# Kernel tuning notes

Hardware: AMD Instinct MI355X
Metric: run time of the kernel (lower is better)

The kernel has to match this reference:

```python
import jax, jax.numpy as jnp
import numpy as np

B, T, D, H, K, M = 2, 2048, 1024, 16, 3, 16384
HD = D // H
SCALE = D * (H ** 0.5)  # faithful to source: n_embd / n_head**(-0.5)


def _normalize(v, axis=-1, eps=1e-12):
    # torch F.normalize: v / max(||v||, eps)
    n = jnp.sqrt(jnp.sum(v * v, axis=axis, keepdims=True))
    return v / jnp.maximum(n, eps)


def setup_inputs() -> dict:
    key = jax.random.key(0)
    ks = jax.random.split(key, 12)
    s = 1.0 / np.sqrt(D)
    return {
        "x": jax.random.normal(ks[0], (B, T, D), jnp.float32),
        "Wq": jax.random.normal(ks[1], (D, D), jnp.float32) * s,
        "bq": jax.random.normal(ks[2], (D,), jnp.float32) * 0.01,
        "Wk": jax.random.normal(ks[3], (D, D), jnp.float32) * s,
        "bk": jax.random.normal(ks[4], (D,), jnp.float32) * 0.01,
        "Wv": jax.random.normal(ks[5], (D, D), jnp.float32) * s,
        "bv": jax.random.normal(ks[6], (D,), jnp.float32) * 0.01,
        "Wo": jax.random.normal(ks[7], (D, D), jnp.float32) * s,
        "bo": jax.random.normal(ks[8], (D,), jnp.float32) * 0.01,
        "gate_bias": jax.random.normal(ks[9], (H, 1, 1), jnp.float32),
        "mem_bank": jax.random.normal(ks[10], (B, M, 2, D), jnp.float32) * s,
        "knn_idx": jax.random.randint(ks[11], (B, T, K), 0, M, jnp.int32),
    }


def reference(x, Wq, bq, Wk, bk, Wv, bv, Wo, bo, gate_bias, mem_bank, knn_idx):
    b, t, d = x.shape
    # projections + L2-normalize q,k (as in source)
    q = _normalize(x @ Wq.T + bq)
    k = _normalize(x @ Wk.T + bk)
    v = x @ Wv.T + bv
    # split heads: b t (h hd) -> b h t hd
    q = q.reshape(b, t, H, HD).transpose(0, 2, 1, 3)
    k = k.reshape(b, t, H, HD).transpose(0, 2, 1, 3)
    v = v.reshape(b, t, H, HD).transpose(0, 2, 1, 3)
    # local causal attention (hand-rolled, dropout is eval no-op)
    qk = jnp.einsum('bhid,bhjd->bhij', q, k) * SCALE  # [b,h,t,t]
    causal = jnp.triu(jnp.ones((t, t), dtype=bool), 1)
    qk = jnp.where(causal, -jnp.inf, qk)
    attn = jax.nn.softmax(qk, axis=-1)
    qkv = jnp.einsum('bhij,bhjd->bhid', attn, v)  # [b,h,t,hd]
    # kNN memory retrieval: gather top-k (key,value) memories per token
    mem = mem_bank[jnp.arange(b)[:, None, None], knn_idx]  # [b,t,k,2,D]
    mem_k = mem[..., 0, :].reshape(b, t, K, H, HD).transpose(0, 3, 1, 2, 4)  # [b,h,t,k,hd]
    mem_v = mem[..., 1, :].reshape(b, t, K, H, HD).transpose(0, 3, 1, 2, 4)
    mem_qk = jnp.einsum('bhtd,bhtkd->bhtk', q.astype(jnp.float32), mem_k) * SCALE
    mem_attn = jax.nn.softmax(mem_qk, axis=-1)
    mem_qkv = jnp.einsum('bhtk,bhtkd->bhtd', mem_attn, mem_v)
    # per-head gated blend, bf16 round-trip (source casts to bfloat16)
    combined = mem_qkv * gate_bias + qkv * (1.0 - gate_bias)  # gate [H,1,1] broadcasts
    combined = combined.astype(jnp.bfloat16).astype(jnp.float32)
    y = combined.transpose(0, 2, 1, 3).reshape(b, t, d)  # b h t hd -> b t D
    return y @ Wo.T + bo
```

## Files before the change

kernel.cpp:

```cpp
#include <hip/hip_runtime.h>
#include <math.h>

#define B_ 2
#define T_ 2048
#define D_ 1024
#define H_ 16
#define HD_ 64
#define M_ 16384
#define SCALE_F 4096.0f
#define LDP 3072
#define ST 72

using short8 = __attribute__((ext_vector_type(8))) short;
using bf16x8 = __attribute__((ext_vector_type(8))) __bf16;
using f32x4  = __attribute__((ext_vector_type(4))) float;

__device__ __forceinline__ unsigned short f2bf(float x){
  unsigned u = __builtin_bit_cast(unsigned, x);
  u += 0x7fffu + ((u >> 16) & 1u);
  return (unsigned short)(u >> 16);
}
__device__ __forceinline__ float bf2f(unsigned short h){
  unsigned u = ((unsigned)h) << 16;
  return __builtin_bit_cast(float, u);
}
__device__ __forceinline__ float bfround(float x){ return bf2f(f2bf(x)); }

__device__ __forceinline__ float wsum(float v){
  #pragma unroll
  for (int off = 32; off; off >>= 1) v += __shfl_xor(v, off);
  return v;
}

__device__ __forceinline__ void ld_g2l16(const unsigned short* g, unsigned short* l){
  __builtin_amdgcn_global_load_lds(
      (const __attribute__((address_space(1))) void*)g,
      (__attribute__((address_space(3))) void*)l, 16, 0, 0);
}

__global__ __launch_bounds__(256)
void cvt_all(const float* __restrict__ x, const float* __restrict__ Wq,
             const float* __restrict__ Wk, const float* __restrict__ Wv,
             const float* __restrict__ Wo,
             unsigned short* __restrict__ Xhi, unsigned short* __restrict__ Xlo,
             unsigned short* __restrict__ Whi, unsigned short* __restrict__ Wlo,
             unsigned short* __restrict__ Wohi)
{
  const int i = blockIdx.x*256 + threadIdx.x;
  const float* src; unsigned short* hi; unsigned short* lo = nullptr; int rel;
  if      (i < 1048576){ src = x;  hi = Xhi;            lo = Xlo;            rel = i; }
  else if (i < 1310720){ src = Wq; hi = Whi;            lo = Wlo;            rel = i - 1048576; }
  else if (i < 1572864){ src = Wk; hi = Whi + 1048576;  lo = Wlo + 1048576;  rel = i - 1310720; }
  else if (i < 1835008){ src = Wv; hi = Whi + 2097152;                       rel = i - 1572864; }
  else                 { src = Wo; hi = Wohi;                                rel = i - 1835008; }
  float4 v = *(const float4*)(src + (size_t)rel*4);
  unsigned short h0=f2bf(v.x), h1=f2bf(v.y), h2=f2bf(v.z), h3=f2bf(v.w);
  uint2 hh; hh.x = (unsigned)h0 | ((unsigned)h1 << 16);
            hh.y = (unsigned)h2 | ((unsigned)h3 << 16);
  *(uint2*)(hi + (size_t)rel*4) = hh;
  if (lo){
    uint2 ll;
    ll.x = (unsigned)f2bf(v.x-bf2f(h0)) | ((unsigned)f2bf(v.y-bf2f(h1)) << 16);
    ll.y = (unsigned)f2bf(v.z-bf2f(h2)) | ((unsigned)f2bf(v.w-bf2f(h3)) << 16);
    *(uint2*)(lo + (size_t)rel*4) = ll;
  }
}

template<bool COMP>
__global__ __launch_bounds__(256)
void gemm_lds(const unsigned short* __restrict__ Ahi_g, const unsigned short* __restrict__ Alo_g,
              const unsigned short* __restrict__ Bhi_g, const unsigned short* __restrict__ Blo_g,
              const float* __restrict__ bias0, const float* __restrict__ bias1,
              const float* __restrict__ bias2,
              float* __restrict__ C, int ldc)
{
  __shared__ __align__(16) unsigned short Ah[128*32];
  __shared__ __align__(16) unsigned short Bh[128*32];
  __shared__ __align__(16) unsigned short Al[COMP ? 128*32 : 8];
  __shared__ __align__(16) unsigned short Bl[COMP ? 128*32 : 8];

  const int tid = threadIdx.x, lane = tid & 63, wv = tid >> 6;
  const int wm = wv >> 1, wn = wv & 1;
  const int mi = lane & 15, quad = lane >> 4;
  const int n0 = blockIdx.x * 128;
  const int m0 = blockIdx.y * 128;
  const int seg = n0 >> 10;
  const float* bias = (seg == 0) ? bias0 : (seg == 1) ? bias1 : bias2;
  const int nw = n0 & 1023;
  const bool comp = COMP && (seg < 2);

  f32x4 acc[4][4];
  #pragma unroll
  for (int a = 0; a < 4; ++a)
    #pragma unroll
    for (int b = 0; b < 4; ++b)
      acc[a][b] = (f32x4){0.f, 0.f, 0.f, 0.f};

  for (int k0 = 0; k0 < 1024; k0 += 32){
    __syncthreads();
    #pragma unroll
    for (int t = 0; t < 2; ++t){
      int j = wv*128 + t*64 + lane;
      int row = j >> 2, c16 = j & 3;
      size_t ga = (size_t)(m0 + row)*1024 + k0 + c16*8;
      size_t gb = (size_t)(n0 + row)*1024 + k0 + c16*8;
      ld_g2l16(Ahi_g + ga, Ah + j*8);
      ld_g2l16(Bhi_g + gb, Bh + j*8);
      if (comp){
        ld_g2l16(Alo_g + ga, Al + j*8);
        ld_g2l16(Blo_g + gb, Bl + j*8);
      }
    }
    __syncthreads();

    bf16x8 ah[4], al[4];
    #pragma unroll
    for (int a = 0; a < 4; ++a){
      int r = wm*64 + a*16 + mi;
      ah[a] = __builtin_bit_cast(bf16x8, *(const short8*)(Ah + r*32 + quad*8));
      if (comp)
        al[a] = __builtin_bit_cast(bf16x8, *(const short8*)(Al + r*32 + quad*8));
    }
    #pragma unroll
    for (int b = 0; b < 4; ++b){
      int r = wn*64 + b*16 + mi;
      bf16x8 bh = __builtin_bit_cast(bf16x8, *(const short8*)(Bh + r*32 + quad*8));
      if (comp){
        bf16x8 bl = __builtin_bit_cast(bf16x8, *(const short8*)(Bl + r*32 + quad*8));
        #pragma unroll
        for (int a = 0; a < 4; ++a){
          acc[a][b] = __builtin_amdgcn_mfma_f32_16x16x32_bf16(al[a], bh, acc[a][b], 0, 0, 0);
          acc[a][b] = __builtin_amdgcn_mfma_f32_16x16x32_bf16(ah[a], bl, acc[a][b], 0, 0, 0);
          acc[a][b] = __builtin_amdgcn_mfma_f32_16x16x32_bf16(ah[a], bh, acc[a][b], 0, 0, 0);
        }
      } else {
        #pragma unroll
        for (int a = 0; a < 4; ++a)
          acc[a][b] = __builtin_amdgcn_mfma_f32_16x16x32_bf16(ah[a], bh, acc[a][b], 0, 0, 0);
      }
    }
  }
  #pragma unroll
  for (int a = 0; a < 4; ++a)
    #pragma unroll
    for (int b = 0; b < 4; ++b)
      #pragma unroll
      for (int r = 0; r < 4; ++r){
        int row  = m0 + wm*64 + a*16 + quad*4 + r;
        int coll = wn*64 + b*16 + mi;
        C[(size_t)row*ldc + n0 + coll] = acc[a][b][r] + bias[nw + coll];
      }
}

__global__ __launch_bounds__(256)
void norm_split(const float* __restrict__ P,
                unsigned short* __restrict__ Qhi, unsigned short* __restrict__ Qlo,
                unsigned short* __restrict__ Khi, unsigned short* __restrict__ Klo,
                unsigned short* __restrict__ Vbf)
{
  const int row = blockIdx.x, tid = threadIdx.x;
  const int bb = row >> 11, t = row & 2047;
  const int lane = tid & 63, wv = tid >> 6;
  const size_t base = (size_t)row * LDP;
  float4 q4 = *(const float4*)(P + base + tid*4);
  float4 k4 = *(const float4*)(P + base + 1024 + tid*4);
  float4 v4 = *(const float4*)(P + base + 2048 + tid*4);
  float sq = wsum(q4.x*q4.x + q4.y*q4.y + q4.z*q4.z + q4.w*q4.w);
  float sk = wsum(k4.x*k4.x + k4.y*k4.y + k4.z*k4.z + k4.w*k4.w);
  __shared__ float rq[4], rk[4];
  if (lane == 0){ rq[wv] = sq; rk[wv] = sk; }
  __syncthreads();
  float cq = 1.f / fmaxf(sqrtf(rq[0]+rq[1]+rq[2]+rq[3]), 1e-12f);
  float ck = 1.f / fmaxf(sqrtf(rk[0]+rk[1]+rk[2]+rk[3]), 1e-12f);
  float qf[4] = {q4.x*cq, q4.y*cq, q4.z*cq, q4.w*cq};
  float kf[4] = {k4.x*ck, k4.y*ck, k4.z*ck, k4.w*ck};

  const int h = tid >> 4, d0 = (tid & 15)*4;
  const size_t ob = ((size_t)(bb*H_ + h)*T_ + t)*64 + d0;

  uint2 qh, ql, kh, kl, vv;
  unsigned short t0,t1,t2,t3;
  t0=f2bf(qf[0]); t1=f2bf(qf[1]); t2=f2bf(qf[2]); t3=f2bf(qf[3]);
  qh.x = t0 | ((unsigned)t1<<16); qh.y = t2 | ((unsigned)t3<<16);
  ql.x = f2bf(qf[0]-bf2f(t0)) | ((unsigned)f2bf(qf[1]-bf2f(t1))<<16);
  ql.y = f2bf(qf[2]-bf2f(t2)) | ((unsigned)f2bf(qf[3]-bf2f(t3))<<16);
  t0=f2bf(kf[0]); t1=f2bf(kf[1]); t2=f2bf(kf[2]); t3=f2bf(kf[3]);
  kh.x = t0 | ((unsigned)t1<<16); kh.y = t2 | ((unsigned)t3<<16);
  kl.x = f2bf(kf[0]-bf2f(t0)) | ((unsigned)f2bf(kf[1]-bf2f(t1))<<16);
  kl.y = f2bf(kf[2]-bf2f(t2)) | ((unsigned)f2bf(kf[3]-bf2f(t3))<<16);
  vv.x = f2bf(v4.x) | ((unsigned)f2bf(v4.y)<<16);
  vv.y = f2bf(v4.z) | ((unsigned)f2bf(v4.w)<<16);
  *(uint2*)(Qhi + ob) = qh;  *(uint2*)(Qlo + ob) = ql;
  *(uint2*)(Khi + ob) = kh;  *(uint2*)(Klo + ob) = kl;
  *(uint2*)(Vbf + ob) = vv;
}

__global__ __launch_bounds__(256)
void attn_knn(const unsigned short* __restrict__ Qhi, const unsigned short* __restrict__ Qlo,
              const unsigned short* __restrict__ Khi_g, const unsigned short* __restrict__ Klo_g,
              const unsigned short* __restrict__ Vbf,
              const float* __restrict__ mem_bank, const int* __restrict__ knn_idx,
              const float* __restrict__ gate_bias, unsigned short* __restrict__ comb)
{
  __shared__ char smpool[36864];
  unsigned short* Kh = (unsigned short*)smpool;
  unsigned short* Kl = (unsigned short*)(smpool + 9216);
  unsigned short* Vt = (unsigned short*)(smpool + 18432);
  unsigned short* Pb = (unsigned short*)(smpool + 27648);
  float* qkvs = (float*)smpool;

  const int bb = blockIdx.z, h = blockIdx.y;
  const int r0 = blockIdx.x * 64;
  const int tid = threadIdx.x, lane = tid & 63, wv = tid >> 6;
  const int mi = lane & 15, quad = lane >> 4;
  const size_t hb = (size_t)(bb*H_ + h)*T_;

  const int qrow = r0 + wv*16 + mi;
  bf16x8 qh[2], ql[2];
  #pragma unroll
  for (int ks = 0; ks < 2; ++ks){
    qh[ks] = __builtin_bit_cast(bf16x8, *(const uint4*)(Qhi + (hb + qrow)*64 + ks*32 + quad*8));
    ql[ks] = __builtin_bit_cast(bf16x8, *(const uint4*)(Qlo + (hb + qrow)*64 + ks*32 + quad*8));
  }

  f32x4 O[4];
  #pragma unroll
  for (int dn = 0; dn < 4; ++dn) O[dn] = (f32x4){0.f,0.f,0.f,0.f};
  float mr = -INFINITY, lr = 0.f;

  const int ntiles = blockIdx.x + 1;
  for (int jt = 0; jt < ntiles; ++jt){
    __syncthreads();
    #pragma unroll
    for (int i = 0; i < 4; ++i){
      int idx = tid + i*256;
      int row = idx >> 4, c4 = idx & 15;
      size_t g = (hb + jt*64 + row)*64 + c4*4;
      *(uint2*)(Kh + row*ST + c4*4) = *(const uint2*)(Khi_g + g);
      *(uint2*)(Kl + row*ST + c4*4) = *(const uint2*)(Klo_g + g);
    }
    #pragma unroll
    for (int i = 0; i < 2; ++i){
      int idx = tid + i*256;
      int rp = idx & 31, d4 = idx >> 5;
      size_t g = (hb + jt*64 + 2*rp)*64 + d4*4;
      ushort4 a = *(const ushort4*)(Vbf + g);
      ushort4 b = *(const ushort4*)(Vbf + g + 64);
      unsigned* vt = (unsigned*)Vt;
      vt[(d4*4+0)*36 + rp] = (unsigned)a.x | ((unsigned)b.x << 16);
      vt[(d4*4+1)*36 + rp] = (unsigned)a.y | ((unsigned)b.y << 16);
      vt[(d4*4+2)*36 + rp] = (unsigned)a.z | ((unsigned)b.z << 16);
      vt[(d4*4+3)*36 + rp] = (unsigned)a.w | ((unsigned)b.w << 16);
    }
    __syncthreads();

    f32x4 st[4];
    #pragma unroll
    for (int mt = 0; mt < 4; ++mt) st[mt] = (f32x4){0.f,0.f,0.f,0.f};
    #pragma unroll
    for (int mt = 0; mt < 4; ++mt){
      int krow = mt*16 + mi;
      #pragma unroll
      for (int ks = 0; ks < 2; ++ks){
        bf16x8 kh = __builtin_bit_cast(bf16x8, *(const short8*)(Kh + krow*ST + ks*32 + quad*8));
        bf16x8 kl = __builtin_bit_cast(bf16x8, *(const short8*)(Kl + krow*ST + ks*32 + quad*8));
        st[mt] = __builtin_amdgcn_mfma_f32_16x16x32_bf16(kl, qh[ks], st[mt], 0, 0, 0);
        st[mt] = __builtin_amdgcn_mfma_f32_16x16x32_bf16(kh, ql[ks], st[mt], 0, 0, 0);
        st[mt] = __builtin_amdgcn_mfma_f32_16x16x32_bf16(kh, qh[ks], st[mt], 0, 0, 0);
      }
    }

    const bool lastt = (jt == ntiles - 1);
    float tmax = -INFINITY;
    #pragma unroll
    for (int mt = 0; mt < 4; ++mt)
      #pragma unroll
      for (int r = 0; r < 4; ++r){
        float s = st[mt][r] * SCALE_F;
        if (lastt){
          int key = jt*64 + mt*16 + quad*4 + r;
          if (key > r0 + wv*16 + mi) s = -INFINITY;
        }
        st[mt][r] = s;
        tmax = fmaxf(tmax, s);
      }
    tmax = fmaxf(tmax, __shfl_xor(tmax, 16));
    tmax = fmaxf(tmax, __shfl_xor(tmax, 32));
    float mnew = fmaxf(mr, tmax);
    float alpha = __expf(mr - mnew);
    mr = mnew;
    float tsum = 0.f;
    #pragma unroll
    for (int mt = 0; mt < 4; ++mt)
      #pragma unroll
      for (int r = 0; r < 4; ++r){
        float p = __expf(st[mt][r] - mnew);
        st[mt][r] = p;
        tsum += p;
      }
    tsum += __shfl_xor(tsum, 16);
    tsum += __shfl_xor(tsum, 32);
    lr = lr*alpha + tsum;

    unsigned short* pw = Pb + wv*1152;
    #pragma unroll
    for (int mt = 0; mt < 4; ++mt){
      uint2 pk;
      pk.x = (unsigned)f2bf(st[mt][0]) | ((unsigned)f2bf(st[mt][1]) << 16);
      pk.y = (unsigned)f2bf(st[mt][2]) | ((unsigned)f2bf(st[mt][3]) << 16);
      *(uint2*)(pw + mi*ST + mt*16 + quad*4) = pk;
    }

    float af[4];
    #pragma unroll
    for (int r = 0; r < 4; ++r) af[r] = __shfl(alpha, quad*4 + r);
    #pragma unroll
    for (int dn = 0; dn < 4; ++dn)
      #pragma unroll
      for (int r = 0; r < 4; ++r) O[dn][r] *= af[r];

    #pragma unroll
    for (int kt = 0; kt < 2; ++kt){
      bf16x8 pf = __builtin_bit_cast(bf16x8, *(const short8*)(pw + mi*ST + kt*32 + quad*8));
      #pragma unroll
      for (int dn = 0; dn < 4; ++dn){
        bf16x8 vf = __builtin_bit_cast(bf16x8, *(const short8*)(Vt + (dn*16 + mi)*ST + kt*32 + quad*8));
        O[dn] = __builtin_amdgcn_mfma_f32_16x16x32_bf16(pf, vf, O[dn], 0, 0, 0);
      }
    }
  }

  __syncthreads();
  float linv[4];
  #pragma unroll
  for (int r = 0; r < 4; ++r) linv[r] = 1.f / __shfl(lr, quad*4 + r);
  #pragma unroll
  for (int dn = 0; dn < 4; ++dn)
    #pragma unroll
    for (int r = 0; r < 4; ++r)
      qkvs[(wv*16 + quad*4 + r)*68 + dn*16 + mi] = O[dn][r] * linv[r];
  __syncthreads();

  const float g = gate_bias[h];
  for (int rr = 0; rr < 16; ++rr){
    int trow = r0 + wv*16 + rr;
    float qd = bf2f(Qhi[(hb + trow)*64 + lane]) + bf2f(Qlo[(hb + trow)*64 + lane]);
    const int* kidx = knn_idx + ((size_t)bb*T_ + trow)*3;
    int idxs[3]; float dts[3]; float mx = -INFINITY;
    #pragma unroll
    for (int kk = 0; kk < 3; ++kk){
      int idx = kidx[kk];
      idxs[kk] = idx;
      const float* mk = mem_bank + (((size_t)bb*M_ + idx)*2 + 0)*D_ + h*HD_;
      float dkk = wsum(qd * mk[lane]) * SCALE_F;
      dts[kk] = dkk;
      mx = fmaxf(mx, dkk);
    }
    float e0 = __expf(dts[0]-mx), e1 = __expf(dts[1]-mx), e2 = __expf(dts[2]-mx);
    float inv = 1.f/(e0+e1+e2);
    const float* mv0 = mem_bank + (((size_t)bb*M_ + idxs[0])*2 + 1)*D_ + h*HD_;
    const float* mv1 = mem_bank + (((size_t)bb*M_ + idxs[1])*2 + 1)*D_ + h*HD_;
    const float* mv2 = mem_bank + (((size_t)bb*M_ + idxs[2])*2 + 1)*D_ + h*HD_;
    float ov = e0*inv*mv0[lane] + e1*inv*mv1[lane] + e2*inv*mv2[lane];
    float qkv = qkvs[(wv*16 + rr)*68 + lane];
    comb[((size_t)bb*T_ + trow)*D_ + h*HD_ + lane] = f2bf(ov*g + qkv*(1.f - g));
  }
}

extern "C" void kernel_launch(void* const* d_in, const int* in_sizes, int n_in,
                              void* d_out, int out_size, void* d_ws, size_t ws_size,
                              hipStream_t stream)
{
  (void)in_sizes; (void)n_in; (void)out_size; (void)ws_size;
  const float* x    = (const float*)d_in[0];
  const float* Wq   = (const float*)d_in[1];
  const float* bq   = (const float*)d_in[2];
  const float* Wk   = (const float*)d_in[3];
  const float* bk   = (const float*)d_in[4];
  const float* Wv   = (const float*)d_in[5];
  const float* bv   = (const float*)d_in[6];
  const float* Wo   = (const float*)d_in[7];
  const float* bo   = (const float*)d_in[8];
  const float* gate = (const float*)d_in[9];
  const float* mem  = (const float*)d_in[10];
  const int*   knn  = (const int*)d_in[11];

  char* ws = (char*)d_ws;
  float*          P    = (float*)ws;
  unsigned short* comb = (unsigned short*)ws;
  unsigned short* Qhi  = (unsigned short*)(ws +  50331648);
  unsigned short* Qlo  = (unsigned short*)(ws +  58720256);
  unsigned short* Khi  = (unsigned short*)(ws +  67108864);
  unsigned short* Klo  = (unsigned short*)(ws +  75497472);
  unsigned short* Vbf  = (unsigned short*)(ws +  83886080);
  unsigned short* Xhi  = (unsigned short*)(ws +  92274688);
  unsigned short* Xlo  = (unsigned short*)(ws + 100663296);
  unsigned short* Whi  = (unsigned short*)(ws + 109051904);
  unsigned short* Wlo  = (unsigned short*)(ws + 115343360);
  unsigned short* Wohi = (unsigned short*)(ws + 119537664);

  cvt_all<<<8192, 256, 0, stream>>>(x, Wq, Wk, Wv, Wo, Xhi, Xlo, Whi, Wlo, Wohi);
  gemm_lds<true><<<dim3(24, 32), 256, 0, stream>>>(Xhi, Xlo, Whi, Wlo, bq, bk, bv, P, LDP);
  norm_split<<<4096, 256, 0, stream>>>(P, Qhi, Qlo, Khi, Klo, Vbf);
  attn_knn<<<dim3(T_/64, H_, B_), 256, 0, stream>>>(Qhi, Qlo, Khi, Klo, Vbf,
                                                    mem, knn, gate, comb);
  gemm_lds<false><<<dim3(8, 32), 256, 0, stream>>>(comb, nullptr, Wohi, nullptr,
                                                   bo, bo, bo, (float*)d_out, D_);
}
```

Measured before the change: 619.4 us.

## Pair complementary causal query tiles per block and vectorize kNN retrieval

Each attention block now processes two query tiles, p and 31-p, so every block does the same amount of causal work. Each loaded K/V tile is also reused by both query sets, which halves K/V global traffic per tile. The kNN memory epilogue is restructured so four lanes share one token, with float4 loads of mem_bank and 16-element vector stores instead of per-lane scalar loads and full wave reductions. The cost is higher register pressure from two Q and O sets, and half as many blocks (512), which lowers parallelism on the device.

```diff
diff --git a/kernel.cpp b/kernel.cpp
--- a/kernel.cpp
+++ b/kernel.cpp
@@ -24,7 +24,6 @@
   unsigned u = ((unsigned)h) << 16;
   return __builtin_bit_cast(float, u);
 }
-__device__ __forceinline__ float bfround(float x){ return bf2f(f2bf(x)); }
 
 __device__ __forceinline__ float wsum(float v){
   #pragma unroll
@@ -195,6 +194,87 @@
   *(uint2*)(Vbf + ob) = vv;
 }
 
+__device__ __forceinline__ void attn_tile(
+    const unsigned short* __restrict__ Kh, const unsigned short* __restrict__ Kl,
+    const unsigned short* __restrict__ Vt, unsigned short* __restrict__ pw,
+    const bf16x8* qh, const bf16x8* ql,
+    f32x4* O, float& mr, float& lr,
+    bool last, int relrow, int mi, int quad)
+{
+  f32x4 st[4];
+  #pragma unroll
+  for (int mt = 0; mt < 4; ++mt) st[mt] = (f32x4){0.f,0.f,0.f,0.f};
+  #pragma unroll
+  for (int mt = 0; mt < 4; ++mt){
+    int krow = mt*16 + mi;
+    #pragma unroll
+    for (int ks = 0; ks < 2; ++ks){
+      bf16x8 kh = __builtin_bit_cast(bf16x8, *(const short8*)(Kh + krow*ST + ks*32 + quad*8));
+      bf16x8 kl = __builtin_bit_cast(bf16x8, *(const short8*)(Kl + krow*ST + ks*32 + quad*8));
+      st[mt] = __builtin_amdgcn_mfma_f32_16x16x32_bf16(kl, qh[ks], st[mt], 0, 0, 0);
+      st[mt] = __builtin_amdgcn_mfma_f32_16x16x32_bf16(kh, ql[ks], st[mt], 0, 0, 0);
+      st[mt] = __builtin_amdgcn_mfma_f32_16x16x32_bf16(kh, qh[ks], st[mt], 0, 0, 0);
+    }
+  }
+
+  float tmax = -INFINITY;
+  #pragma unroll
+  for (int mt = 0; mt < 4; ++mt)
+    #pragma unroll
+    for (int r = 0; r < 4; ++r){
+      float s = st[mt][r] * SCALE_F;
+      if (last){
+        int key = mt*16 + quad*4 + r;
+        if (key > relrow) s = -INFINITY;
+      }
+      st[mt][r] = s;
+      tmax = fmaxf(tmax, s);
+    }
+  tmax = fmaxf(tmax, __shfl_xor(tmax, 16));
+  tmax = fmaxf(tmax, __shfl_xor(tmax, 32));
+  float mnew = fmaxf(mr, tmax);
+  float alpha = __expf(mr - mnew);
+  mr = mnew;
+  float tsum = 0.f;
+  #pragma unroll
+  for (int mt = 0; mt < 4; ++mt)
+    #pragma unroll
+    for (int r = 0; r < 4; ++r){
+      float p = __expf(st[mt][r] - mnew);
+      st[mt][r] = p;
+      tsum += p;
+    }
+  tsum += __shfl_xor(tsum, 16);
+  tsum += __shfl_xor(tsum, 32);
+  lr = lr*alpha + tsum;
+
+  #pragma unroll
+  for (int mt = 0; mt < 4; ++mt){
+    uint2 pk;
+    pk.x = (unsigned)f2bf(st[mt][0]) | ((unsigned)f2bf(st[mt][1]) << 16);
+    pk.y = (unsigned)f2bf(st[mt][2]) | ((unsigned)f2bf(st[mt][3]) << 16);
+    *(uint2*)(pw + mi*ST + mt*16 + quad*4) = pk;
+  }
+
+  float af[4];
+  #pragma unroll
+  for (int r = 0; r < 4; ++r) af[r] = __shfl(alpha, quad*4 + r);
+  #pragma unroll
+  for (int dn = 0; dn < 4; ++dn)
+    #pragma unroll
+    for (int r = 0; r < 4; ++r) O[dn][r] *= af[r];
+
+  #pragma unroll
+  for (int kt = 0; kt < 2; ++kt){
+    bf16x8 pf = __builtin_bit_cast(bf16x8, *(const short8*)(pw + mi*ST + kt*32 + quad*8));
+    #pragma unroll
+    for (int dn = 0; dn < 4; ++dn){
+      bf16x8 vf = __builtin_bit_cast(bf16x8, *(const short8*)(Vt + (dn*16 + mi)*ST + kt*32 + quad*8));
+      O[dn] = __builtin_amdgcn_mfma_f32_16x16x32_bf16(pf, vf, O[dn], 0, 0, 0);
+    }
+  }
+}
+
 __global__ __launch_bounds__(256)
 void attn_knn(const unsigned short* __restrict__ Qhi, const unsigned short* __restrict__ Qlo,
               const unsigned short* __restrict__ Khi_g, const unsigned short* __restrict__ Klo_g,
@@ -210,25 +290,32 @@
   float* qkvs = (float*)smpool;
 
   const int bb = blockIdx.z, h = blockIdx.y;
-  const int r0 = blockIdx.x * 64;
+  const int p = blockIdx.x;
+  const int jA = p, jB = 31 - p;
   const int tid = threadIdx.x, lane = tid & 63, wv = tid >> 6;
   const int mi = lane & 15, quad = lane >> 4;
+  const int relrow = wv*16 + mi;
   const size_t hb = (size_t)(bb*H_ + h)*T_;
-
-  const int qrow = r0 + wv*16 + mi;
-  bf16x8 qh[2], ql[2];
+  unsigned short* pw = Pb + wv*1152;
+
+  bf16x8 qhA[2], qlA[2], qhB[2], qlB[2];
   #pragma unroll
   for (int ks = 0; ks < 2; ++ks){
-    qh[ks] = __builtin_bit_cast(bf16x8, *(const uint4*)(Qhi + (hb + qrow)*64 + ks*32 + quad*8));
-    ql[ks] = __builtin_bit_cast(bf16x8, *(const uint4*)(Qlo + (hb + qrow)*64 + ks*32 + quad*8));
-  }
-
-  f32x4 O[4];
-  #pragma unroll
-  for (int dn = 0; dn < 4; ++dn) O[dn] = (f32x4){0.f,0.f,0.f,0.f};
-  float mr = -INFINITY, lr = 0.f;
-
-  const int ntiles = blockIdx.x + 1;
+    qhA[ks] = __builtin_bit_cast(bf16x8, *(const uint4*)(Qhi + (hb + jA*64 + relrow)*64 + ks*32 + quad*8));
+    qlA[ks] = __builtin_bit_cast(bf16x8, *(const uint4*)(Qlo + (hb + jA*64 + relrow)*64 + ks*32 + quad*8));
+    qhB[ks] = __builtin_bit_cast(bf16x8, *(const uint4*)(Qhi + (hb + jB*64 + relrow)*64 + ks*32 + quad*8));
+    qlB[ks] = __builtin_bit_cast(bf16x8, *(const uint4*)(Qlo + (hb + jB*64 + relrow)*64 + ks*32 + quad*8));
+  }
+
+  f32x4 OA[4], OB[4];
+  #pragma unroll
+  for (int dn = 0; dn < 4; ++dn){
+    OA[dn] = (f32x4){0.f,0.f,0.f,0.f};
+    OB[dn] = (f32x4){0.f,0.f,0.f,0.f};
+  }
+  float mA = -INFINITY, lA = 0.f, mB = -INFINITY, lB = 0.f;
+
+  const int ntiles = jB + 1;
   for (int jt = 0; jt < ntiles; ++jt){
     __syncthreads();
     #pragma unroll
@@ -254,116 +341,104 @@
     }
     __syncthreads();
 
-    f32x4 st[4];
-    #pragma unroll
-    for (int mt = 0; mt < 4; ++mt) st[mt] = (f32x4){0.f,0.f,0.f,0.f};
-    #pragma unroll
-    for (int mt = 0; mt < 4; ++mt){
-      int krow = mt*16 + mi;
-      #pragma unroll
-      for (int ks = 0; ks < 2; ++ks){
-        bf16x8 kh = __builtin_bit_cast(bf16x8, *(const short8*)(Kh + krow*ST + ks*32 + quad*8));
-        bf16x8 kl = __builtin_bit_cast(bf16x8, *(const short8*)(Kl + krow*ST + ks*32 + quad*8));
-        st[mt] = __builtin_amdgcn_mfma_f32_16x16x32_bf16(kl, qh[ks], st[mt], 0, 0, 0);
-        st[mt] = __builtin_amdgcn_mfma_f32_16x16x32_bf16(kh, ql[ks], st[mt], 0, 0, 0);
-        st[mt] = __builtin_amdgcn_mfma_f32_16x16x32_bf16(kh, qh[ks], st[mt], 0, 0, 0);
-      }
-    }
-
-    const bool lastt = (jt == ntiles - 1);
-    float tmax = -INFINITY;
-    #pragma unroll
-    for (int mt = 0; mt < 4; ++mt)
+    if (jt <= jA)
+      attn_tile(Kh, Kl, Vt, pw, qhA, qlA, OA, mA, lA, jt == jA, relrow, mi, quad);
+    attn_tile(Kh, Kl, Vt, pw, qhB, qlB, OB, mB, lB, jt == jB, relrow, mi, quad);
+  }
+
+  __syncthreads();
+  {
+    float liA[4], liB[4];
+    #pragma unroll
+    for (int r = 0; r < 4; ++r){
+      liA[r] = 1.f / __shfl(lA, quad*4 + r);
+      liB[r] = 1.f / __shfl(lB, quad*4 + r);
+    }
+    #pragma unroll
+    for (int dn = 0; dn < 4; ++dn)
       #pragma unroll
       for (int r = 0; r < 4; ++r){
-        float s = st[mt][r] * SCALE_F;
-        if (lastt){
-          int key = jt*64 + mt*16 + quad*4 + r;
-          if (key > r0 + wv*16 + mi) s = -INFINITY;
-        }
-        st[mt][r] = s;
-        tmax = fmaxf(tmax, s);
-      }
-    tmax = fmaxf(tmax, __shfl_xor(tmax, 16));
-    tmax = fmaxf(tmax, __shfl_xor(tmax, 32));
-    float mnew = fmaxf(mr, tmax);
-    float alpha = __expf(mr - mnew);
-    mr = mnew;
-    float tsum = 0.f;
-    #pragma unroll
-    for (int mt = 0; mt < 4; ++mt)
+        qkvs[(      wv*16 + quad*4 + r)*68 + dn*16 + mi] = OA[dn][r] * liA[r];
+        qkvs[(64 +  wv*16 + quad*4 + r)*68 + dn*16 + mi] = OB[dn][r] * liB[r];
+      }
+  }
+  __syncthreads();
+
+  const float g = gate_bias[h];
+  const float gq = 1.f - g;
+  const int sub = lane & 3;
+  const int grp = tid >> 2;
+  const int base = lane & 60;
+
+  #pragma unroll
+  for (int it = 0; it < 2; ++it){
+    const int jq = it ? jB : jA;
+    const int trow = jq*64 + grp;
+    const int lrow = it*64 + grp;
+    const int* kidx = knn_idx + ((size_t)bb*T_ + trow)*3;
+    int myidx = 0;
+    if (sub < 3) myidx = kidx[sub];
+
+    float qf[16];
+    {
+      const unsigned short* qp = Qhi + (hb + trow)*64 + sub*16;
+      const unsigned short* lp = Qlo + (hb + trow)*64 + sub*16;
+      unsigned short hs[16], ls[16];
+      *(uint4*)hs     = *(const uint4*)qp;
+      *(uint4*)(hs+8) = *(const uint4*)(qp+8);
+      *(uint4*)ls     = *(const uint4*)lp;
+      *(uint4*)(ls+8) = *(const uint4*)(lp+8);
       #pragma unroll
-      for (int r = 0; r < 4; ++r){
-        float p = __expf(st[mt][r] - mnew);
-        st[mt][r] = p;
-        tsum += p;
-      }
-    tsum += __shfl_xor(tsum, 16);
-    tsum += __shfl_xor(tsum, 32);
-    lr = lr*alpha + tsum;
-
-    unsigned short* pw = Pb + wv*1152;
-    #pragma unroll
-    for (int mt = 0; mt < 4; ++mt){
-      uint2 pk;
-      pk.x = (unsigned)f2bf(st[mt][0]) | ((unsigned)f2bf(st[mt][1]) << 16);
-      pk.y = (unsigned)f2bf(st[mt][2]) | ((unsigned)f2bf(st[mt][3]) << 16);
-      *(uint2*)(pw + mi*ST + mt*16 + quad*4) = pk;
-    }
-
-    float af[4];
-    #pragma unroll
-    for (int r = 0; r < 4; ++r) af[r] = __shfl(alpha, quad*4 + r);
-    #pragma unroll
-    for (int dn = 0; dn < 4; ++dn)
+      for (int j = 0; j < 16; ++j) qf[j] = bf2f(hs[j]) + bf2f(ls[j]);
+    }
+
+    int idxs[3]; float dts[3]; float mx = -INFINITY;
+    #pragma unroll
+    for (int kk = 0; kk < 3; ++kk){
+      int idx = __shfl(myidx, base + kk);
+      idxs[kk] = idx;
+      const float* mk = mem_bank + (((size_t)bb*M_ + idx)*2 + 0)*D_ + h*HD_ + sub*16;
+      float dsum = 0.f;
       #pragma unroll
-      for (int r = 0; r < 4; ++r) O[dn][r] *= af[r];
-
-    #pragma unroll
-    for (int kt = 0; kt < 2; ++kt){
-      bf16x8 pf = __builtin_bit_cast(bf16x8, *(const short8*)(pw + mi*ST + kt*32 + quad*8));
-      #pragma unroll
-      for (int dn = 0; dn < 4; ++dn){
-        bf16x8 vf = __builtin_bit_cast(bf16x8, *(const short8*)(Vt + (dn*16 + mi)*ST + kt*32 + quad*8));
-        O[dn] = __builtin_amdgcn_mfma_f32_16x16x32_bf16(pf, vf, O[dn], 0, 0, 0);
-      }
-    }
-  }
-
-  __syncthreads();
-  float linv[4];
-  #pragma unroll
-  for (int r = 0; r < 4; ++r) linv[r] = 1.f / __shfl(lr, quad*4 + r);
-  #pragma unroll
-  for (int dn = 0; dn < 4; ++dn)
-    #pragma unroll
-    for (int r = 0; r < 4; ++r)
-      qkvs[(wv*16 + quad*4 + r)*68 + dn*16 + mi] = O[dn][r] * linv[r];
-  __syncthreads();
-
-  const float g = gate_bias[h];
-  for (int rr = 0; rr < 16; ++rr){
-    int trow = r0 + wv*16 + rr;
-    float qd = bf2f(Qhi[(hb + trow)*64 + lane]) + bf2f(Qlo[(hb + trow)*64 + lane]);
-    const int* kidx = knn_idx + ((size_t)bb*T_ + trow)*3;
-    int idxs[3]; float dts[3]; float mx = -INFINITY;
-    #pragma unroll
-    for (int kk = 0; kk < 3; ++kk){
-      int idx = kidx[kk];
-      idxs[kk] = idx;
-      const float* mk = mem_bank + (((size_t)bb*M_ + idx)*2 + 0)*D_ + h*HD_;
-      float dkk = wsum(qd * mk[lane]) * SCALE_F;
-      dts[kk] = dkk;
-      mx = fmaxf(mx, dkk);
+      for (int j4 = 0; j4 < 4; ++j4){
+        float4 m4 = *(const float4*)(mk + j4*4);
+        dsum += qf[j4*4+0]*m4.x + qf[j4*4+1]*m4.y + qf[j4*4+2]*m4.z + qf[j4*4+3]*m4.w;
+      }
+      dsum += __shfl_xor(dsum, 1);
+      dsum += __shfl_xor(dsum, 2);
+      dsum *= SCALE_F;
+      dts[kk] = dsum;
+      mx = fmaxf(mx, dsum);
     }
     float e0 = __expf(dts[0]-mx), e1 = __expf(dts[1]-mx), e2 = __expf(dts[2]-mx);
     float inv = 1.f/(e0+e1+e2);
-    const float* mv0 = mem_bank + (((size_t)bb*M_ + idxs[0])*2 + 1)*D_ + h*HD_;
-    const float* mv1 = mem_bank + (((size_t)bb*M_ + idxs[1])*2 + 1)*D_ + h*HD_;
-    const float* mv2 = mem_bank + (((size_t)bb*M_ + idxs[2])*2 + 1)*D_ + h*HD_;
-    float ov = e0*inv*mv0[lane] + e1*inv*mv1[lane] + e2*inv*mv2[lane];
-    float qkv = qkvs[(wv*16 + rr)*68 + lane];
-    comb[((size_t)bb*T_ + trow)*D_ + h*HD_ + lane] = f2bf(ov*g + qkv*(1.f - g));
+    float w[3] = {e0*inv, e1*inv, e2*inv};
+
+    float ov[16];
+    #pragma unroll
+    for (int j = 0; j < 16; ++j) ov[j] = 0.f;
+    #pragma unroll
+    for (int kk = 0; kk < 3; ++kk){
+      const float* mv = mem_bank + (((size_t)bb*M_ + idxs[kk])*2 + 1)*D_ + h*HD_ + sub*16;
+      #pragma unroll
+      for (int j4 = 0; j4 < 4; ++j4){
+        float4 m4 = *(const float4*)(mv + j4*4);
+        ov[j4*4+0] += w[kk]*m4.x;
+        ov[j4*4+1] += w[kk]*m4.y;
+        ov[j4*4+2] += w[kk]*m4.z;
+        ov[j4*4+3] += w[kk]*m4.w;
+      }
+    }
+
+    unsigned short os[16];
+    #pragma unroll
+    for (int j = 0; j < 16; ++j){
+      float qkv = qkvs[lrow*68 + sub*16 + j];
+      os[j] = f2bf(ov[j]*g + qkv*gq);
+    }
+    unsigned short* op = comb + ((size_t)bb*T_ + trow)*D_ + h*HD_ + sub*16;
+    *(uint4*)op     = *(uint4*)os;
+    *(uint4*)(op+8) = *(uint4*)(os+8);
   }
 }
 
@@ -402,8 +477,8 @@
   cvt_all<<<8192, 256, 0, stream>>>(x, Wq, Wk, Wv, Wo, Xhi, Xlo, Whi, Wlo, Wohi);
   gemm_lds<true><<<dim3(24, 32), 256, 0, stream>>>(Xhi, Xlo, Whi, Wlo, bq, bk, bv, P, LDP);
   norm_split<<<4096, 256, 0, stream>>>(P, Qhi, Qlo, Khi, Klo, Vbf);
-  attn_knn<<<dim3(T_/64, H_, B_), 256, 0, stream>>>(Qhi, Qlo, Khi, Klo, Vbf,
-                                                    mem, knn, gate, comb);
+  attn_knn<<<dim3(T_/128, H_, B_), 256, 0, stream>>>(Qhi, Qlo, Khi, Klo, Vbf,
+                                                     mem, knn, gate, comb);
   gemm_lds<false><<<dim3(8, 32), 256, 0, stream>>>(comb, nullptr, Wohi, nullptr,
                                                    bo, bo, bo, (float*)d_out, D_);
 }
```

Result: faster. 586.0 us (-5.4%).
